# Optimization experiments

Measured on AMD Instinct MI355X. Metric: run time of the kernel, lower is better.

## Reference

```python
import jax, jax.numpy as jnp
import numpy as np

RATIO = 0.8

def _sage(x, src, dst, mask, Wl, bl, Wr, n):
    # PyG SAGEConv (mean aggr): lin_l(mean_j x_j) + lin_r(x_i); bias on lin_l only
    msg = x[src] * mask[:, None]                               # [E, d]
    agg = jax.ops.segment_sum(msg, dst, num_segments=n)       # [n, d]
    cnt = jax.ops.segment_sum(mask, dst, num_segments=n)      # [n]
    mean = agg / jnp.maximum(cnt, 1.0)[:, None]
    return mean @ Wl + bl + x @ Wr

def _topk(x, src, dst, mask, w, Bg, Npg):
    # PyG TopKPooling: score = tanh(x.w/||w||); keep top ceil(ratio*N) per graph; x' = x[perm]*score
    K = int(np.ceil(RATIO * Npg))
    score = jnp.tanh((x @ w) / jnp.linalg.norm(w))             # [Bg*Npg]
    vals, idx = jax.lax.top_k(score.reshape(Bg, Npg), K)       # [Bg, K]
    perm = (idx + (jnp.arange(Bg) * Npg)[:, None]).reshape(-1)
    x_new = x[perm] * vals.reshape(-1, 1)                      # [Bg*K, d]
    new_id = jnp.full((Bg * Npg,), -1, jnp.int32).at[perm].set(jnp.arange(Bg * K, dtype=jnp.int32))
    s2 = new_id[src]; d2 = new_id[dst]
    valid = mask * ((s2 >= 0) & (d2 >= 0)).astype(x.dtype)     # filter_adj as a mask
    return x_new, jnp.maximum(s2, 0), jnp.maximum(d2, 0), valid, K

def _readout(x, Bg, K):
    # global_max_pool || global_mean_pool (equal-sized graphs -> reshape)
    xr = x.reshape(Bg, K, x.shape[-1])
    return jnp.concatenate([xr.max(axis=1), xr.mean(axis=1)], axis=-1)

def _forward(x, edge_index, params, Bg, Npg):
    (Wl1, bl1, Wr1, pw1, Wl2, bl2, Wr2, pw2, Wl3, bl3, Wr3, pw3,
     W1, b1, W2, b2, W3, b3) = params
    src = edge_index[0]; dst = edge_index[1]
    mask = jnp.ones(src.shape, x.dtype)
    n = Bg * Npg
    h = jax.nn.relu(_sage(x, src, dst, mask, Wl1, bl1, Wr1, n))
    h, src, dst, mask, K = _topk(h, src, dst, mask, pw1, Bg, Npg)
    x1 = _readout(h, Bg, K)
    h = jax.nn.relu(_sage(h, src, dst, mask, Wl2, bl2, Wr2, Bg * K))
    h, src, dst, mask, K = _topk(h, src, dst, mask, pw2, Bg, K)
    x2 = _readout(h, Bg, K)
    h = jax.nn.relu(_sage(h, src, dst, mask, Wl3, bl3, Wr3, Bg * K))
    h, src, dst, mask, K = _topk(h, src, dst, mask, pw3, Bg, K)
    x3 = _readout(h, Bg, K)
    s = x1 + x2 + x3                                           # [Bg, 256]
    s = jax.nn.relu(s @ W1 + b1)
    s = jax.nn.relu(s @ W2 + b2)                               # dropout: eval mode no-op
    return jax.nn.sigmoid(s @ W3 + b3).squeeze(-1)             # [Bg]

def setup_inputs() -> dict:
    key = jax.random.key(0)
    ks = jax.random.split(key, 24)
    B, N, DEG, D = 64, 1024, 16, 128
    x = jax.random.normal(ks[0], (B * N, D), jnp.float32)
    off = (jnp.arange(B) * N)[:, None]
    src = (jax.random.randint(ks[1], (B, N * DEG), 0, N) + off).reshape(-1)
    dst = (jax.random.randint(ks[2], (B, N * DEG), 0, N) + off).reshape(-1)
    edge_index = jnp.stack([src, dst]).astype(jnp.int32)
    s = 1.0 / np.sqrt(D)
    def w(k, shp, sc): return jax.random.normal(k, shp, jnp.float32) * sc
    inp = dict(x=x, edge_index=edge_index)
    for i, k0 in zip((1, 2, 3), (3, 7, 11)):
        inp[f'Wl{i}'] = w(ks[k0], (D, D), s)
        inp[f'bl{i}'] = jnp.zeros((D,), jnp.float32)
        inp[f'Wr{i}'] = w(ks[k0 + 1], (D, D), s)
        inp[f'pw{i}'] = w(ks[k0 + 2], (D,), s)
    inp['W1'] = w(ks[15], (256, 128), 1.0 / np.sqrt(256)); inp['b1'] = jnp.zeros((128,), jnp.float32)
    inp['W2'] = w(ks[16], (128, 64), 1.0 / np.sqrt(128)); inp['b2'] = jnp.zeros((64,), jnp.float32)
    inp['W3'] = w(ks[17], (64, 1), 1.0 / np.sqrt(64)); inp['b3'] = jnp.zeros((1,), jnp.float32)
    inp['B'] = B; inp['N'] = N
    return inp

def reference(x, edge_index, Wl1, bl1, Wr1, pw1, Wl2, bl2, Wr2, pw2, Wl3, bl3, Wr3, pw3, W1, b1, W2, b2, W3, b3, B, N):
    params = (Wl1, bl1, Wr1, pw1, Wl2, bl2, Wr2, pw2, Wl3, bl3, Wr3, pw3, W1, b1, W2, b2, W3, b3)
    return _forward(x, edge_index, params, B, N)
```

## Files before the change

### kernel.cpp

```cpp
#include <hip/hip_runtime.h>
#include <math.h>

#define D       128
#define NGRAPH  64
#define N0      1024
#define NE      (1<<20)
#define EPG     (NE/NGRAPH)
#define NTOT    (NGRAPH*N0)
#define MAXSLOT 128

__device__ float g_h[NTOT*D];
__device__ float g_h2[NTOT*D];
__device__ unsigned short g_mh[NTOT*D];
__device__ unsigned short g_ml[NTOT*D];
__device__ unsigned short g_xh[NTOT*D];
__device__ unsigned short g_xl[NTOT*D];
__device__ unsigned short g_wbh[3*128*256];
__device__ unsigned short g_wbl[3*128*256];
__device__ int   g_esrc[NE];
__device__ int   g_edst[NE];
__device__ int   g_adj[NTOT*MAXSLOT];
__device__ int   g_cnt[NTOT];
__device__ float g_dot[NTOT];
__device__ float g_pwnorm[3];
__device__ int   g_selidx[NGRAPH*820];
__device__ float g_selval[NGRAPH*820];
__device__ int   g_newid[NTOT];
__device__ float g_pool[NGRAPH*8*256];
__device__ float g_s[NGRAPH*256];

typedef __attribute__((ext_vector_type(8))) short bf16x8;
typedef __attribute__((ext_vector_type(8))) unsigned short ushort8;
typedef __attribute__((ext_vector_type(4))) float f32x4;

__device__ inline unsigned short f2bf_rne(float f) {
    unsigned u = __float_as_uint(f);
    u += 0x7FFF + ((u >> 16) & 1);
    return (unsigned short)(u >> 16);
}
__device__ inline void split2(float v, unsigned short& h, unsigned short& l) {
    h = f2bf_rne(v);
    l = f2bf_rne(v - __uint_as_float((unsigned)h << 16));
}

__global__ void k_init_s() {
    int i = blockIdx.x * 256 + threadIdx.x;
    if (i < NGRAPH * 256) g_s[i] = 0.f;
}

__global__ void k_prep_w(const float* __restrict__ Wl1, const float* __restrict__ Wr1,
                         const float* __restrict__ Wl2, const float* __restrict__ Wr2,
                         const float* __restrict__ Wl3, const float* __restrict__ Wr3) {
    int t = blockIdx.x * 256 + threadIdx.x;
    int r = t >> 15, rem = t & 32767;
    int c = rem >> 8, k = rem & 255;
    const float* WlR = (r == 0) ? Wl1 : (r == 1) ? Wl2 : Wl3;
    const float* WrR = (r == 0) ? Wr1 : (r == 1) ? Wr2 : Wr3;
    float v = (k < 128) ? WlR[k * 128 + c] : WrR[(k - 128) * 128 + c];
    split2(v, g_wbh[t], g_wbl[t]);
}

__global__ void k_norms(const float* __restrict__ p1, const float* __restrict__ p2,
                        const float* __restrict__ p3) {
    int r = blockIdx.x, lane = threadIdx.x;
    const float* p = (r == 0) ? p1 : (r == 1) ? p2 : p3;
    float a = p[lane], b = p[lane + 64];
    float s = a * a + b * b;
    for (int off = 32; off; off >>= 1) s += __shfl_xor(s, off);
    if (lane == 0) g_pwnorm[r] = sqrtf(s);
}

__global__ void k_prep_x(const float* __restrict__ x) {
    int t = blockIdx.x * 256 + threadIdx.x;
    float4 v = ((const float4*)x)[t];
    ushort4 h4, l4;
    split2(v.x, h4.x, l4.x); split2(v.y, h4.y, l4.y);
    split2(v.z, h4.z, l4.z); split2(v.w, h4.w, l4.w);
    ((ushort4*)g_xh)[t] = h4;
    ((ushort4*)g_xl)[t] = l4;
}

__global__ void k_zero_cnt(int n) {
    int stride = gridDim.x * blockDim.x;
    for (int i = blockIdx.x * blockDim.x + threadIdx.x; i < n; i += stride) {
        g_cnt[i] = 0; g_dot[i] = 0.f;
    }
}

__global__ void k_build_adj(const int* __restrict__ ei, int use_input) {
    const int* es = use_input ? ei : g_esrc;
    const int* ed = use_input ? (ei + NE) : g_edst;
    int b = blockIdx.x;
    int j = b >> 3;
    int g = (b & 7) + 8 * (j >> 6);
    int ib = j & 63;
    int e = g * EPG + ib * 256 + threadIdx.x;
    int d = ed[e];
    if (d >= 0) {
        int s = es[e];
        int slot = atomicAdd(&g_cnt[d], 1);
        if (slot < MAXSLOT) g_adj[d * MAXSLOT + slot] = s;
    }
}

__global__ __launch_bounds__(256) void k_aggregate(const float* __restrict__ x_in,
                                                   int use_input, int M, int BPG) {
    const float* X = use_input ? x_in : g_h;
    int b = blockIdx.x;
    int j = b >> 3;
    int g = (b & 7) + 8 * (j / BPG);
    int ib = j % BPG;
    int wid = threadIdx.x >> 6, lane = threadIdx.x & 63;
    int half = lane >> 5, li = lane & 31;
    int local = ib * 8 + wid * 2 + half;
    int node = g * M + local;
    int cnt = (local < M) ? min(g_cnt[node], MAXSLOT) : 0;
    int cnt2 = max(cnt, __shfl_xor(cnt, 32));
    float ax = 0.f, ay = 0.f, az = 0.f, aw = 0.f;
    const float4* Xp = (const float4*)X;
    int abase = node * MAXSLOT;
    for (int base = 0; base < cnt2; base += 32) {
        int a = (base + li < cnt) ? g_adj[abase + base + li] : -1;
        int mm = min(cnt2 - base, 32);
        int mmr = (mm + 3) & ~3;
        for (int i = 0; i < mmr; i += 4) {
            int s0 = __shfl(a, half * 32 + i + 0);
            int s1 = __shfl(a, half * 32 + i + 1);
            int s2 = __shfl(a, half * 32 + i + 2);
            int s3 = __shfl(a, half * 32 + i + 3);
            float4 v0 = Xp[(size_t)max(s0, 0) * 32 + li];
            float4 v1 = Xp[(size_t)max(s1, 0) * 32 + li];
            float4 v2 = Xp[(size_t)max(s2, 0) * 32 + li];
            float4 v3 = Xp[(size_t)max(s3, 0) * 32 + li];
            float m0 = (s0 >= 0) ? 1.f : 0.f, m1 = (s1 >= 0) ? 1.f : 0.f;
            float m2 = (s2 >= 0) ? 1.f : 0.f, m3 = (s3 >= 0) ? 1.f : 0.f;
            ax += m0 * v0.x + m1 * v1.x + m2 * v2.x + m3 * v3.x;
            ay += m0 * v0.y + m1 * v1.y + m2 * v2.y + m3 * v3.y;
            az += m0 * v0.z + m1 * v1.z + m2 * v2.z + m3 * v3.z;
            aw += m0 * v0.w + m1 * v1.w + m2 * v2.w + m3 * v3.w;
        }
    }
    if (local < M) {
        float inv = 1.f / (float)max(cnt, 1);
        ushort4 h4, l4;
        split2(ax * inv, h4.x, l4.x); split2(ay * inv, h4.y, l4.y);
        split2(az * inv, h4.z, l4.z); split2(aw * inv, h4.w, l4.w);
        *(ushort4*)&g_mh[(size_t)node * 128 + li * 4] = h4;
        *(ushort4*)&g_ml[(size_t)node * 128 + li * 4] = l4;
    }
}

__global__ __launch_bounds__(256, 2) void k_gemm(int r,
                                                 const float* __restrict__ bl,
                                                 const float* __restrict__ pw) {
    __shared__ __align__(16) unsigned short sa_hi[128 * 40];
    __shared__ __align__(16) unsigned short sa_lo[128 * 40];
    __shared__ __align__(16) unsigned short sb_hi[128 * 40];
    __shared__ __align__(16) unsigned short sb_lo[128 * 40];
    const unsigned short* Wbh = g_wbh + r * 32768;
    const unsigned short* Wbl = g_wbl + r * 32768;
    int tid = threadIdx.x;
    int row0 = blockIdx.x * 128;
    int wid = tid >> 6, lane = tid & 63;
    int wr = wid >> 1, wc = wid & 1;
    int lrow = lane & 15, kgrp = lane >> 4;

    f32x4 acc[4][4];
#pragma unroll
    for (int mi = 0; mi < 4; mi++)
#pragma unroll
        for (int ni = 0; ni < 4; ni++)
#pragma unroll
            for (int q = 0; q < 4; q++) acc[mi][ni][q] = 0.f;

    for (int kc = 0; kc < 256; kc += 32) {
        const unsigned short* Ah = (kc < 128) ? g_mh : g_xh;
        const unsigned short* Al = (kc < 128) ? g_ml : g_xl;
        int kloc = kc & 127;
        __syncthreads();
#pragma unroll
        for (int i = 0; i < 2; i++) {
            int f = tid + i * 256;
            int row = f >> 2, kq = f & 3;
            size_t src = (size_t)(row0 + row) * 128 + kloc + kq * 8;
            *(ushort8*)&sa_hi[row * 40 + kq * 8] = *(const ushort8*)&Ah[src];
            *(ushort8*)&sa_lo[row * 40 + kq * 8] = *(const ushort8*)&Al[src];
        }
#pragma unroll
        for (int i = 0; i < 2; i++) {
            int f = tid + i * 256;
            int c = f >> 2, kq = f & 3;
            size_t src = (size_t)c * 256 + kc + kq * 8;
            *(ushort8*)&sb_hi[c * 40 + kq * 8] = *(const ushort8*)&Wbh[src];
            *(ushort8*)&sb_lo[c * 40 + kq * 8] = *(const ushort8*)&Wbl[src];
        }
        __syncthreads();
        bf16x8 ah[4], al[4], bh[4], blo[4];
#pragma unroll
        for (int mi = 0; mi < 4; mi++) {
            int rr = wr * 64 + mi * 16 + lrow;
            ah[mi] = *(const bf16x8*)&sa_hi[rr * 40 + kgrp * 8];
            al[mi] = *(const bf16x8*)&sa_lo[rr * 40 + kgrp * 8];
        }
#pragma unroll
        for (int ni = 0; ni < 4; ni++) {
            int c = wc * 64 + ni * 16 + lrow;
            bh[ni]  = *(const bf16x8*)&sb_hi[c * 40 + kgrp * 8];
            blo[ni] = *(const bf16x8*)&sb_lo[c * 40 + kgrp * 8];
        }
#pragma unroll
        for (int mi = 0; mi < 4; mi++)
#pragma unroll
            for (int ni = 0; ni < 4; ni++) {
                acc[mi][ni] = __builtin_amdgcn_mfma_f32_16x16x32_bf16(ah[mi], bh[ni],  acc[mi][ni], 0, 0, 0);
                acc[mi][ni] = __builtin_amdgcn_mfma_f32_16x16x32_bf16(ah[mi], blo[ni], acc[mi][ni], 0, 0, 0);
                acc[mi][ni] = __builtin_amdgcn_mfma_f32_16x16x32_bf16(al[mi], bh[ni],  acc[mi][ni], 0, 0, 0);
            }
    }
    float pwv[4];
#pragma unroll
    for (int ni = 0; ni < 4; ni++) pwv[ni] = pw[wc * 64 + ni * 16 + lrow];
#pragma unroll
    for (int mi = 0; mi < 4; mi++) {
        float dotq[4] = {0.f, 0.f, 0.f, 0.f};
#pragma unroll
        for (int ni = 0; ni < 4; ni++) {
            int c = wc * 64 + ni * 16 + lrow;
            float b = bl[c];
#pragma unroll
            for (int q = 0; q < 4; q++) {
                float v = fmaxf(acc[mi][ni][q] + b, 0.f);
                g_h2[(size_t)(row0 + wr * 64 + mi * 16 + kgrp * 4 + q) * 128 + c] = v;
                dotq[q] += v * pwv[ni];
            }
        }
#pragma unroll
        for (int q = 0; q < 4; q++) {
            float dv = dotq[q];
            dv += __shfl_xor(dv, 1); dv += __shfl_xor(dv, 2);
            dv += __shfl_xor(dv, 4); dv += __shfl_xor(dv, 8);
            if (lrow == 0)
                atomicAdd(&g_dot[row0 + wr * 64 + mi * 16 + kgrp * 4 + q], dv);
        }
    }
}

__global__ void k_topk(int M, int K, int rr) {
    __shared__ float sc[1024];
    __shared__ int   id[1024];
    int g = blockIdx.x, tid = threadIdx.x;
    float invn = 1.f / g_pwnorm[rr];
    for (int i = tid; i < 1024; i += 512) {
        sc[i] = (i < M) ? g_dot[g * M + i] : -INFINITY;
        id[i] = i;
    }
    for (int i = tid; i < M; i += 512) g_newid[g * M + i] = -1;
    __syncthreads();
    for (int k = 2; k <= 1024; k <<= 1) {
        for (int j = k >> 1; j > 0; j >>= 1) {
            for (int i = tid; i < 1024; i += 512) {
                int ixj = i ^ j;
                if (ixj > i) {
                    bool desc = ((i & k) == 0);
                    float a = sc[i], b = sc[ixj];
                    bool sw = desc ? (a < b) : (a > b);
                    if (sw) {
                        sc[i] = b; sc[ixj] = a;
                        int t = id[i]; id[i] = id[ixj]; id[ixj] = t;
                    }
                }
            }
            __syncthreads();
        }
    }
    for (int j = tid; j < K; j += 512) {
        int li = id[j];
        g_selidx[g * K + j] = g * M + li;
        g_selval[g * K + j] = tanhf(sc[j] * invn);
        g_newid[g * M + li] = g * K + j;
    }
}

__global__ void k_gather_pool(int K) {
    int g = blockIdx.x, chunk = blockIdx.y;
    int cs = (K + 7) / 8;
    int j0 = chunk * cs, j1 = min(K, j0 + cs);
    int tid = threadIdx.x;
    int c = tid & 127, half = tid >> 7;
    float mx = -INFINITY, sm = 0.f;
    for (int j = j0 + half; j < j1; j += 2) {
        int srcRow = g_selidx[g * K + j];
        float v = g_h2[(size_t)srcRow * 128 + c] * g_selval[g * K + j];
        size_t o = (size_t)(g * K + j) * 128 + c;
        g_h[o] = v;
        split2(v, g_xh[o], g_xl[o]);
        mx = fmaxf(mx, v); sm += v;
    }
    __shared__ float smx[256], ssm[256];
    smx[tid] = mx; ssm[tid] = sm;
    __syncthreads();
    if (half == 0) {
        mx = fmaxf(mx, smx[tid + 128]);
        sm += ssm[tid + 128];
        g_pool[(g * 8 + chunk) * 256 + c] = mx;
        g_pool[(g * 8 + chunk) * 256 + 128 + c] = sm;
    }
}

__global__ void k_pool_combine(int K) {
    int g = blockIdx.x, tid = threadIdx.x;
    if (tid < 128) {
        float mx = -INFINITY;
        for (int ch = 0; ch < 8; ch++) mx = fmaxf(mx, g_pool[(g * 8 + ch) * 256 + tid]);
        g_s[g * 256 + tid] += mx;
    } else {
        int c = tid - 128;
        float sm = 0.f;
        for (int ch = 0; ch < 8; ch++) sm += g_pool[(g * 8 + ch) * 256 + 128 + c];
        g_s[g * 256 + 128 + c] += sm / (float)K;
    }
}

__global__ void k_remap(const int* __restrict__ ei, int use_input) {
    const int* es = use_input ? ei : g_esrc;
    const int* ed = use_input ? (ei + NE) : g_edst;
    int b = blockIdx.x;
    int j = b >> 3;
    int g = (b & 7) + 8 * (j >> 6);
    int ib = j & 63;
    int e = g * EPG + ib * 256 + threadIdx.x;
    int d = ed[e];
    if (d < 0) { g_edst[e] = -1; return; }
    int ns = g_newid[es[e]];
    int nd = g_newid[d];
    if (ns < 0 || nd < 0) g_edst[e] = -1;
    else { g_esrc[e] = ns; g_edst[e] = nd; }
}

__global__ void k_mlp(const float* __restrict__ W1, const float* __restrict__ b1,
                      const float* __restrict__ W2, const float* __restrict__ b2,
                      const float* __restrict__ W3, const float* __restrict__ b3,
                      float* __restrict__ out) {
    int g = blockIdx.x, tid = threadIdx.x;
    __shared__ float h1[128], h2[64], red[128];
    float a = 0.f;
    for (int k = 0; k < 256; k++) a += g_s[g * 256 + k] * W1[k * 128 + tid];
    h1[tid] = fmaxf(a + b1[tid], 0.f);
    __syncthreads();
    if (tid < 64) {
        float a2 = 0.f;
        for (int k = 0; k < 128; k++) a2 += h1[k] * W2[k * 64 + tid];
        h2[tid] = fmaxf(a2 + b2[tid], 0.f);
    }
    __syncthreads();
    red[tid] = (tid < 64) ? h2[tid] * W3[tid] : 0.f;
    __syncthreads();
    for (int s = 64; s > 0; s >>= 1) {
        if (tid < s) red[tid] += red[tid + s];
        __syncthreads();
    }
    if (tid == 0) {
        float z = red[0] + b3[0];
        out[g] = 1.f / (1.f + expf(-z));
    }
}

extern "C" void kernel_launch(void* const* d_in, const int* in_sizes, int n_in,
                              void* d_out, int out_size, void* d_ws, size_t ws_size,
                              hipStream_t stream) {
    const float* x  = (const float*)d_in[0];
    const int*   ei = (const int*)d_in[1];
    const float* Wl[3] = {(const float*)d_in[2], (const float*)d_in[6],  (const float*)d_in[10]};
    const float* bl[3] = {(const float*)d_in[3], (const float*)d_in[7],  (const float*)d_in[11]};
    const float* Wr[3] = {(const float*)d_in[4], (const float*)d_in[8],  (const float*)d_in[12]};
    const float* pw[3] = {(const float*)d_in[5], (const float*)d_in[9],  (const float*)d_in[13]};
    const float* W1 = (const float*)d_in[14]; const float* b1 = (const float*)d_in[15];
    const float* W2 = (const float*)d_in[16]; const float* b2 = (const float*)d_in[17];
    const float* W3 = (const float*)d_in[18]; const float* b3 = (const float*)d_in[19];
    float* out = (float*)d_out;

    const int Ms[3] = {1024, 820, 656};
    const int Ks[3] = {820, 656, 525};

    k_init_s<<<64, 256, 0, stream>>>();
    k_prep_w<<<384, 256, 0, stream>>>(Wl[0], Wr[0], Wl[1], Wr[1], Wl[2], Wr[2]);
    k_norms<<<3, 64, 0, stream>>>(pw[0], pw[1], pw[2]);
    k_prep_x<<<NTOT * D / 4 / 256, 256, 0, stream>>>(x);

    for (int r = 0; r < 3; r++) {
        int M = Ms[r], K = Ks[r];
        int n = NGRAPH * M;
        int BPG = (M + 7) / 8;
        int use_input = (r == 0) ? 1 : 0;
        k_zero_cnt<<<256, 256, 0, stream>>>(n);
        k_build_adj<<<NGRAPH * (EPG / 256), 256, 0, stream>>>(ei, use_input);
        k_aggregate<<<NGRAPH * BPG, 256, 0, stream>>>(x, use_input, M, BPG);
        k_gemm<<<n / 128, 256, 0, stream>>>(r, bl[r], pw[r]);
        k_topk<<<NGRAPH, 512, 0, stream>>>(M, K, r);
        k_gather_pool<<<dim3(NGRAPH, 8), 256, 0, stream>>>(K);
        k_pool_combine<<<NGRAPH, 256, 0, stream>>>(K);
        if (r < 2) k_remap<<<NGRAPH * (EPG / 256), 256, 0, stream>>>(ei, use_input);
    }
    k_mlp<<<NGRAPH, 128, 0, stream>>>(W1, b1, W2, b2, W3, b3, out);
}
```

Measured before the change: 613.7 us.

## Build adjacency once in shared memory and compact it per pooling round

Replaces the per-round edge remap and global-atomic adjacency rebuild with two steps. Round one builds per-graph adjacency lists using shared-memory atomics in one block per graph. Later rounds compact the surviving neighbours of each kept node with a wavefront ballot, ping-ponging between two adjacency buffers. Zeroing of the dot buffer moves into the aggregate kernel, and the pool-combine step folds into the MLP kernel, dropping several launches and full passes over the million-edge list. Per-node capacity drops to 64 slots, so nodes with more neighbours than that would be silently truncated.

```diff
diff --git a/kernel.cpp b/kernel.cpp
--- a/kernel.cpp
+++ b/kernel.cpp
@@ -7,7 +7,7 @@
 #define NE      (1<<20)
 #define EPG     (NE/NGRAPH)
 #define NTOT    (NGRAPH*N0)
-#define MAXSLOT 128
+#define ASLOT   64
 
 __device__ float g_h[NTOT*D];
 __device__ float g_h2[NTOT*D];
@@ -17,18 +17,16 @@
 __device__ unsigned short g_xl[NTOT*D];
 __device__ unsigned short g_wbh[3*128*256];
 __device__ unsigned short g_wbl[3*128*256];
-__device__ int   g_esrc[NE];
-__device__ int   g_edst[NE];
-__device__ int   g_adj[NTOT*MAXSLOT];
-__device__ int   g_cnt[NTOT];
+__device__ int   g_adjA[NTOT*ASLOT];
+__device__ int   g_adjB[NTOT*ASLOT];
+__device__ int   g_cntA[NTOT];
+__device__ int   g_cntB[NTOT];
 __device__ float g_dot[NTOT];
 __device__ float g_pwnorm[3];
 __device__ int   g_selidx[NGRAPH*820];
 __device__ float g_selval[NGRAPH*820];
 __device__ int   g_newid[NTOT];
-__device__ float g_pool[NGRAPH*8*256];
-__device__ float g_s[NGRAPH*256];
-
+__device__ float g_pool[3*NGRAPH*8*256];
 typedef __attribute__((ext_vector_type(8))) short bf16x8;
 typedef __attribute__((ext_vector_type(8))) unsigned short ushort8;
 typedef __attribute__((ext_vector_type(4))) float f32x4;
@@ -41,11 +39,6 @@
 __device__ inline void split2(float v, unsigned short& h, unsigned short& l) {
     h = f2bf_rne(v);
     l = f2bf_rne(v - __uint_as_float((unsigned)h << 16));
-}
-
-__global__ void k_init_s() {
-    int i = blockIdx.x * 256 + threadIdx.x;
-    if (i < NGRAPH * 256) g_s[i] = 0.f;
 }
 
 __global__ void k_prep_w(const float* __restrict__ Wl1, const float* __restrict__ Wr1,
@@ -80,32 +73,47 @@
     ((ushort4*)g_xl)[t] = l4;
 }
 
-__global__ void k_zero_cnt(int n) {
-    int stride = gridDim.x * blockDim.x;
-    for (int i = blockIdx.x * blockDim.x + threadIdx.x; i < n; i += stride) {
-        g_cnt[i] = 0; g_dot[i] = 0.f;
-    }
-}
-
-__global__ void k_build_adj(const int* __restrict__ ei, int use_input) {
-    const int* es = use_input ? ei : g_esrc;
-    const int* ed = use_input ? (ei + NE) : g_edst;
-    int b = blockIdx.x;
-    int j = b >> 3;
-    int g = (b & 7) + 8 * (j >> 6);
-    int ib = j & 63;
-    int e = g * EPG + ib * 256 + threadIdx.x;
-    int d = ed[e];
-    if (d >= 0) {
-        int s = es[e];
-        int slot = atomicAdd(&g_cnt[d], 1);
-        if (slot < MAXSLOT) g_adj[d * MAXSLOT + slot] = s;
-    }
+__global__ __launch_bounds__(1024) void k_badj0(const int* __restrict__ ei) {
+    __shared__ int s_fill[N0];
+    int g = blockIdx.x, tid = threadIdx.x;
+    s_fill[tid] = 0;
+    __syncthreads();
+    int e0 = g * EPG;
+#pragma unroll
+    for (int i = 0; i < EPG / 1024; i++) {
+        int e = e0 + i * 1024 + tid;
+        int s = ei[e];
+        int d = ei[NE + e];
+        int slot = atomicAdd(&s_fill[d - g * N0], 1);
+        if (slot < ASLOT) g_adjA[(size_t)d * ASLOT + slot] = s;
+    }
+    __syncthreads();
+    g_cntA[g * N0 + tid] = min(s_fill[tid], ASLOT);
+}
+
+__global__ __launch_bounds__(256) void k_compact(int n_new, int dir) {
+    int wid = threadIdx.x >> 6, lane = threadIdx.x & 63;
+    int nj = blockIdx.x * 4 + wid;
+    if (nj >= n_new) return;
+    int old = g_selidx[nj];
+    const int* adjO = dir ? g_adjB : g_adjA;
+    const int* cntO = dir ? g_cntB : g_cntA;
+    int* adjN = dir ? g_adjA : g_adjB;
+    int* cntN = dir ? g_cntA : g_cntB;
+    int cnt = cntO[old];
+    int m = -1;
+    if (lane < cnt) m = g_newid[adjO[(size_t)old * ASLOT + lane]];
+    unsigned long long mask = __ballot(m >= 0);
+    int pos = __popcll(mask & ((1ull << lane) - 1ull));
+    if (m >= 0) adjN[(size_t)nj * ASLOT + pos] = m;
+    if (lane == 0) cntN[nj] = __popcll(mask);
 }
 
 __global__ __launch_bounds__(256) void k_aggregate(const float* __restrict__ x_in,
-                                                   int use_input, int M, int BPG) {
+                                                   int use_input, int ab, int M, int BPG) {
     const float* X = use_input ? x_in : g_h;
+    const int* adj = ab ? g_adjB : g_adjA;
+    const int* cntp = ab ? g_cntB : g_cntA;
     int b = blockIdx.x;
     int j = b >> 3;
     int g = (b & 7) + 8 * (j / BPG);
@@ -114,13 +122,13 @@
     int half = lane >> 5, li = lane & 31;
     int local = ib * 8 + wid * 2 + half;
     int node = g * M + local;
-    int cnt = (local < M) ? min(g_cnt[node], MAXSLOT) : 0;
+    int cnt = (local < M) ? cntp[node] : 0;
     int cnt2 = max(cnt, __shfl_xor(cnt, 32));
     float ax = 0.f, ay = 0.f, az = 0.f, aw = 0.f;
     const float4* Xp = (const float4*)X;
-    int abase = node * MAXSLOT;
+    size_t abase = (size_t)node * ASLOT;
     for (int base = 0; base < cnt2; base += 32) {
-        int a = (base + li < cnt) ? g_adj[abase + base + li] : -1;
+        int a = (base + li < cnt) ? adj[abase + base + li] : -1;
         int mm = min(cnt2 - base, 32);
         int mmr = (mm + 3) & ~3;
         for (int i = 0; i < mmr; i += 4) {
@@ -147,6 +155,7 @@
         split2(az * inv, h4.z, l4.z); split2(aw * inv, h4.w, l4.w);
         *(ushort4*)&g_mh[(size_t)node * 128 + li * 4] = h4;
         *(ushort4*)&g_ml[(size_t)node * 128 + li * 4] = l4;
+        if (li == 0) g_dot[node] = 0.f;
     }
 }
 
@@ -281,7 +290,7 @@
     }
 }
 
-__global__ void k_gather_pool(int K) {
+__global__ void k_gather_pool(int K, int rr) {
     int g = blockIdx.x, chunk = blockIdx.y;
     int cs = (K + 7) / 8;
     int j0 = chunk * cs, j1 = min(K, j0 + cs);
@@ -302,58 +311,42 @@
     if (half == 0) {
         mx = fmaxf(mx, smx[tid + 128]);
         sm += ssm[tid + 128];
-        g_pool[(g * 8 + chunk) * 256 + c] = mx;
-        g_pool[(g * 8 + chunk) * 256 + 128 + c] = sm;
-    }
-}
-
-__global__ void k_pool_combine(int K) {
-    int g = blockIdx.x, tid = threadIdx.x;
-    if (tid < 128) {
-        float mx = -INFINITY;
-        for (int ch = 0; ch < 8; ch++) mx = fmaxf(mx, g_pool[(g * 8 + ch) * 256 + tid]);
-        g_s[g * 256 + tid] += mx;
-    } else {
-        int c = tid - 128;
-        float sm = 0.f;
-        for (int ch = 0; ch < 8; ch++) sm += g_pool[(g * 8 + ch) * 256 + 128 + c];
-        g_s[g * 256 + 128 + c] += sm / (float)K;
-    }
-}
-
-__global__ void k_remap(const int* __restrict__ ei, int use_input) {
-    const int* es = use_input ? ei : g_esrc;
-    const int* ed = use_input ? (ei + NE) : g_edst;
-    int b = blockIdx.x;
-    int j = b >> 3;
-    int g = (b & 7) + 8 * (j >> 6);
-    int ib = j & 63;
-    int e = g * EPG + ib * 256 + threadIdx.x;
-    int d = ed[e];
-    if (d < 0) { g_edst[e] = -1; return; }
-    int ns = g_newid[es[e]];
-    int nd = g_newid[d];
-    if (ns < 0 || nd < 0) g_edst[e] = -1;
-    else { g_esrc[e] = ns; g_edst[e] = nd; }
+        g_pool[((rr * NGRAPH + g) * 8 + chunk) * 256 + c] = mx;
+        g_pool[((rr * NGRAPH + g) * 8 + chunk) * 256 + 128 + c] = sm;
+    }
 }
 
 __global__ void k_mlp(const float* __restrict__ W1, const float* __restrict__ b1,
                       const float* __restrict__ W2, const float* __restrict__ b2,
                       const float* __restrict__ W3, const float* __restrict__ b3,
-                      float* __restrict__ out) {
+                      float* __restrict__ out, int K0, int K1, int K2) {
     int g = blockIdx.x, tid = threadIdx.x;
-    __shared__ float h1[128], h2[64], red[128];
+    __shared__ float s_sh[256], h1[128], h2v[64], red[128];
+    float Kf[3] = {(float)K0, (float)K1, (float)K2};
+    float accmax = 0.f, accmean = 0.f;
+    for (int r = 0; r < 3; r++) {
+        float mx = -INFINITY, sm = 0.f;
+        for (int ch = 0; ch < 8; ch++) {
+            const float* p = &g_pool[((r * NGRAPH + g) * 8 + ch) * 256];
+            mx = fmaxf(mx, p[tid]);
+            sm += p[128 + tid];
+        }
+        accmax += mx;
+        accmean += sm / Kf[r];
+    }
+    s_sh[tid] = accmax; s_sh[128 + tid] = accmean;
+    __syncthreads();
     float a = 0.f;
-    for (int k = 0; k < 256; k++) a += g_s[g * 256 + k] * W1[k * 128 + tid];
+    for (int k = 0; k < 256; k++) a += s_sh[k] * W1[k * 128 + tid];
     h1[tid] = fmaxf(a + b1[tid], 0.f);
     __syncthreads();
     if (tid < 64) {
         float a2 = 0.f;
         for (int k = 0; k < 128; k++) a2 += h1[k] * W2[k * 64 + tid];
-        h2[tid] = fmaxf(a2 + b2[tid], 0.f);
-    }
-    __syncthreads();
-    red[tid] = (tid < 64) ? h2[tid] * W3[tid] : 0.f;
+        h2v[tid] = fmaxf(a2 + b2[tid], 0.f);
+    }
+    __syncthreads();
+    red[tid] = (tid < 64) ? h2v[tid] * W3[tid] : 0.f;
     __syncthreads();
     for (int s = 64; s > 0; s >>= 1) {
         if (tid < s) red[tid] += red[tid + s];
@@ -382,7 +375,6 @@
     const int Ms[3] = {1024, 820, 656};
     const int Ks[3] = {820, 656, 525};
 
-    k_init_s<<<64, 256, 0, stream>>>();
     k_prep_w<<<384, 256, 0, stream>>>(Wl[0], Wr[0], Wl[1], Wr[1], Wl[2], Wr[2]);
     k_norms<<<3, 64, 0, stream>>>(pw[0], pw[1], pw[2]);
     k_prep_x<<<NTOT * D / 4 / 256, 256, 0, stream>>>(x);
@@ -391,15 +383,16 @@
         int M = Ms[r], K = Ks[r];
         int n = NGRAPH * M;
         int BPG = (M + 7) / 8;
-        int use_input = (r == 0) ? 1 : 0;
-        k_zero_cnt<<<256, 256, 0, stream>>>(n);
-        k_build_adj<<<NGRAPH * (EPG / 256), 256, 0, stream>>>(ei, use_input);
-        k_aggregate<<<NGRAPH * BPG, 256, 0, stream>>>(x, use_input, M, BPG);
+        int ab = (r == 1) ? 1 : 0;
+        if (r == 0)
+            k_badj0<<<NGRAPH, 1024, 0, stream>>>(ei);
+        else
+            k_compact<<<(n + 3) / 4, 256, 0, stream>>>(n, r - 1);
+        k_aggregate<<<NGRAPH * BPG, 256, 0, stream>>>(x, (r == 0) ? 1 : 0, ab, M, BPG);
         k_gemm<<<n / 128, 256, 0, stream>>>(r, bl[r], pw[r]);
         k_topk<<<NGRAPH, 512, 0, stream>>>(M, K, r);
-        k_gather_pool<<<dim3(NGRAPH, 8), 256, 0, stream>>>(K);
-        k_pool_combine<<<NGRAPH, 256, 0, stream>>>(K);
-        if (r < 2) k_remap<<<NGRAPH * (EPG / 256), 256, 0, stream>>>(ei, use_input);
-    }
-    k_mlp<<<NGRAPH, 128, 0, stream>>>(W1, b1, W2, b2, W3, b3, out);
-}
+        k_gather_pool<<<dim3(NGRAPH, 8), 256, 0, stream>>>(K, r);
+    }
+    k_mlp<<<NGRAPH, 128, 0, stream>>>(W1, b1, W2, b2, W3, b3, out,
+                                      Ks[0], Ks[1], Ks[2]);
+}
```

Result: faster. 510.3 us, median of 2 (-16.8%).
